# Kernel optimization log

Measured on AMD Instinct MI355X. Metric: run time of the kernel, lower is better.

Reference implementation:

```python
import jax, jax.numpy as jnp
import numpy as np

N, E = 50000, 640000
FEAT, EMB, HID, B = 128, 128, 512, 32


def setup_inputs() -> dict:
    key = jax.random.key(0)
    ks = jax.random.split(key, 12)
    def w(k, shape, fan_in):
        return jax.random.normal(k, shape, dtype=jnp.float32) / np.sqrt(fan_in)
    return {
        "x": jax.random.normal(ks[0], (N, FEAT), dtype=jnp.float32),
        "edge_index": jax.random.randint(ks[1], (2, E), 0, N, dtype=jnp.int64),
        "last_hidden": jax.random.normal(ks[2], (1, B, HID), dtype=jnp.float32),
        "W1_rel": w(ks[3], (FEAT, EMB), FEAT),
        "W1_root": w(ks[4], (FEAT, EMB), FEAT),
        "b1": jnp.zeros((EMB,), dtype=jnp.float32),
        "W2_rel": w(ks[5], (EMB, EMB), EMB),
        "W2_root": w(ks[6], (EMB, EMB), EMB),
        "b2": jnp.zeros((EMB,), dtype=jnp.float32),
        "Wp": w(ks[7], (HID, EMB), HID),
        "bp": jnp.zeros((EMB,), dtype=jnp.float32),
    }


def _rgcn(h, src, dst, W_rel, W_root, b):
    # transform-then-gather (N < E so cheaper): messages along edges src->dst
    msg = (h @ W_rel)[src]                                   # [E, emb]
    agg = jax.ops.segment_sum(msg, dst, num_segments=N)      # [N, emb]
    deg = jax.ops.segment_sum(jnp.ones((E,), h.dtype), dst, num_segments=N)
    agg = agg / jnp.maximum(deg, 1.0)[:, None]               # mean aggregation (PyG RGCNConv default)
    return agg + h @ W_root + b


def reference(x, edge_index, last_hidden, W1_rel, W1_root, b1, W2_rel, W2_root, b2, Wp, bp):
    src, dst = edge_index[0], edge_index[1]
    h = jax.nn.relu(_rgcn(x, src, dst, W1_rel, W1_root, b1))   # [N, emb]
    h = jax.nn.relu(_rgcn(h, src, dst, W2_rel, W2_root, b2))   # [N, emb]
    message_embed = (last_hidden @ Wp + bp)[0]                 # squeeze(0) -> [B, emb]
    scores = h @ message_embed.T                               # [N, B]
    return jax.nn.log_softmax(scores, axis=0)
```

## Files before the change

### kernel.cpp

```cpp
#include <hip/hip_runtime.h>
#include <hip/hip_bf16.h>

#define N_NODES 50000
#define N_EDGES 640000
#define DUMMY   N_NODES
#define PAD_SSRC 990000

typedef __attribute__((ext_vector_type(8))) short short8;
typedef __attribute__((ext_vector_type(4))) float floatx4;

__device__ __forceinline__ float bf2f(unsigned short u) {
    return __uint_as_float(((unsigned int)u) << 16);
}
__device__ __forceinline__ unsigned short f2bf(float x) {
    unsigned int u = __float_as_uint(x);
    u = (u + 0x7fffu + ((u >> 16) & 1u)) >> 16;
    return (unsigned short)u;
}
__device__ __forceinline__ unsigned char f2f8(float x) {
    int pk = __builtin_amdgcn_cvt_pk_fp8_f32(x, x, 0, false);
    return (unsigned char)(pk & 0xff);
}
__device__ __forceinline__ unsigned int pk4_fp8(float x0, float x1, float x2, float x3) {
    int v = __builtin_amdgcn_cvt_pk_fp8_f32(x0, x1, 0, false);
    v = __builtin_amdgcn_cvt_pk_fp8_f32(x2, x3, v, true);
    return (unsigned int)v;
}
__device__ __forceinline__ unsigned int pk2_bf16(float lo, float hi) {
    return (unsigned int)f2bf(lo) | ((unsigned int)f2bf(hi) << 16);
}

__global__ void __launch_bounds__(256) prep_k(const float* __restrict__ W0,
                                              const float* __restrict__ W1,
                                              const float* __restrict__ W2,
                                              const float* __restrict__ W3,
                                              unsigned short* __restrict__ T0,
                                              unsigned short* __restrict__ T1,
                                              unsigned short* __restrict__ T2,
                                              unsigned short* __restrict__ T3,
                                              int* __restrict__ cnt,
                                              const float* __restrict__ lh,
                                              const float* __restrict__ Wp,
                                              const float* __restrict__ bp,
                                              unsigned short* __restrict__ meb,
                                              unsigned short* __restrict__ ssrc,
                                              unsigned char* __restrict__ tbf,
                                              int* __restrict__ total,
                                              const int* __restrict__ dst,
                                              int* __restrict__ rank) {
    int b = blockIdx.x, tid = threadIdx.x;
    bool is_hist;
    int idx;
    if (b < 4414) { is_hist = ((b & 1) == 0); idx = b >> 1; }
    else          { is_hist = true;            idx = 2207 + (b - 4414); }
    if (is_hist) {
        int e = idx * 256 + tid;
        int d = dst[e];
        int r = atomicAdd(&cnt[d], 1);
        rank[e] = (r << 16) | d;
        return;
    }
    int s = idx;
    if (s < 256) {
        int i2 = s * 256 + tid;
        int w = i2 >> 14;
        int r = i2 & 16383;
        int n = r >> 7, k = r & 127;
        const float* W = (w == 0) ? W0 : (w == 1) ? W1 : (w == 2) ? W2 : W3;
        unsigned short* T = (w == 0) ? T0 : (w == 1) ? T1 : (w == 2) ? T2 : T3;
        T[r] = f2bf(W[k * 128 + n]);
    } else if (s < 272) {
        int o = (s - 256) * 256 + tid;
        int i = o >> 7, c = o & 127;
        float acc = bp[c];
        const float4* lr = (const float4*)(lh + i * 512);
        #pragma unroll 4
        for (int k4 = 0; k4 < 128; k4++) {
            float4 v = lr[k4];
            acc += v.x * Wp[(4 * k4 + 0) * 128 + c] + v.y * Wp[(4 * k4 + 1) * 128 + c]
                 + v.z * Wp[(4 * k4 + 2) * 128 + c] + v.w * Wp[(4 * k4 + 3) * 128 + c];
        }
        meb[o] = f2bf(acc);
    } else if (s < 2206) {
        int i = (s - 272) * 256 + tid;
        if (i < PAD_SSRC / 2) ((unsigned int*)ssrc)[i] = 0xC350C350u;
    } else {
        if (tid < 32) ((unsigned int*)(tbf + (size_t)DUMMY * 128))[tid] = 0;
        else if (tid == 32) *total = 0;
    }
}

#define EPI_LD 132
__device__ __forceinline__ void gemm_dual_body32(int bid, int tid, const short8 a[4],
                                                 const unsigned short* __restrict__ BtRel,
                                                 const unsigned short* __restrict__ BtRoot,
                                                 unsigned char* __restrict__ Trel,
                                                 unsigned short* __restrict__ Rootb,
                                                 int M, float* __restrict__ epi) {
    int wid = tid >> 6, lane = tid & 63;
    int rh = (wid >> 1) * 16;
    int ch = (wid & 1) * 64;
    int m = lane & 15, g = lane >> 4;
    floatx4 accR[4], accO[4];
    #pragma unroll
    for (int ct = 0; ct < 4; ct++) {
        accR[ct] = (floatx4)(0.f);
        accO[ct] = (floatx4)(0.f);
    }
    #pragma unroll
    for (int ct = 0; ct < 4; ct++) {
        const unsigned short* br = BtRel  + (size_t)(ch + ct * 16 + m) * 128 + g * 8;
        const unsigned short* bo = BtRoot + (size_t)(ch + ct * 16 + m) * 128 + g * 8;
        short8 bR[4], bO[4];
        #pragma unroll
        for (int kt = 0; kt < 4; kt++) {
            bR[kt] = *(const short8*)(br + kt * 32);
            bO[kt] = *(const short8*)(bo + kt * 32);
        }
        #pragma unroll
        for (int kt = 0; kt < 4; kt++) {
            accR[ct] = __builtin_amdgcn_mfma_f32_16x16x32_bf16(a[kt], bR[kt], accR[ct], 0, 0, 0);
            accO[ct] = __builtin_amdgcn_mfma_f32_16x16x32_bf16(a[kt], bO[kt], accO[ct], 0, 0, 0);
        }
    }
    int r0 = bid * 32;
    #pragma unroll
    for (int ct = 0; ct < 4; ct++)
        #pragma unroll
        for (int rg = 0; rg < 4; rg++)
            epi[(rh + g * 4 + rg) * EPI_LD + ch + ct * 16 + m] = accR[ct][rg];
    __syncthreads();
    {
        int lr = tid >> 3, c0 = (tid & 7) * 16;
        int ro = r0 + lr;
        const float* row = epi + lr * EPI_LD + c0;
        if (ro < M) {
            uint4 w;
            w.x = pk4_fp8(row[0],  row[1],  row[2],  row[3]);
            w.y = pk4_fp8(row[4],  row[5],  row[6],  row[7]);
            w.z = pk4_fp8(row[8],  row[9],  row[10], row[11]);
            w.w = pk4_fp8(row[12], row[13], row[14], row[15]);
            *(uint4*)(Trel + (size_t)ro * 128 + c0) = w;
        }
    }
    __syncthreads();
    #pragma unroll
    for (int ct = 0; ct < 4; ct++)
        #pragma unroll
        for (int rg = 0; rg < 4; rg++)
            epi[(rh + g * 4 + rg) * EPI_LD + ch + ct * 16 + m] = accO[ct][rg];
    __syncthreads();
    {
        int lr = tid >> 3, c0 = (tid & 7) * 16;
        int ro = r0 + lr;
        const float* row = epi + lr * EPI_LD + c0;
        if (ro < M) {
            uint4 w0, w1;
            w0.x = pk2_bf16(row[0],  row[1]);
            w0.y = pk2_bf16(row[2],  row[3]);
            w0.z = pk2_bf16(row[4],  row[5]);
            w0.w = pk2_bf16(row[6],  row[7]);
            w1.x = pk2_bf16(row[8],  row[9]);
            w1.y = pk2_bf16(row[10], row[11]);
            w1.z = pk2_bf16(row[12], row[13]);
            w1.w = pk2_bf16(row[14], row[15]);
            *(uint4*)(Rootb + (size_t)ro * 128 + c0) = w0;
            *(uint4*)(Rootb + (size_t)ro * 128 + c0 + 8) = w1;
        }
    }
}

__global__ void __launch_bounds__(256) allocgemm_k(const int* __restrict__ cnt,
                                                   int* __restrict__ prow,
                                                   int* __restrict__ total,
                                                   const float* __restrict__ A,
                                                   const unsigned short* __restrict__ BtRel,
                                                   const unsigned short* __restrict__ BtRoot,
                                                   unsigned char* __restrict__ Trel,
                                                   unsigned short* __restrict__ Rootb) {
    __shared__ float epi[32 * EPI_LD];
    __shared__ int sm[256];
    __shared__ int base_s;
    if (blockIdx.x < 196) {
        int t = threadIdx.x;
        int i = blockIdx.x * 256 + t;
        int pc = (i < N_NODES) ? ((cnt[i] + 7) & ~7) : 0;
        sm[t] = pc;
        __syncthreads();
        for (int off = 1; off < 256; off <<= 1) {
            int v = (t >= off) ? sm[t - off] : 0;
            __syncthreads();
            sm[t] += v;
            __syncthreads();
        }
        if (t == 255) base_s = atomicAdd(total, sm[255]);
        __syncthreads();
        if (i < N_NODES) prow[i] = base_s + sm[t] - pc;
    } else {
        int bid = blockIdx.x - 196, tid = threadIdx.x;
        int wid = tid >> 6, lane = tid & 63;
        int r0 = bid * 32 + (wid >> 1) * 16;
        int m = lane & 15, g = lane >> 4;
        int row = r0 + m;
        int rowc = (row < N_NODES) ? row : (N_NODES - 1);
        short8 a[4];
        #pragma unroll
        for (int kt = 0; kt < 4; kt++) {
            const float* p = A + (size_t)rowc * 128 + kt * 32 + g * 8;
            float4 v0 = *(const float4*)p;
            float4 v1 = *(const float4*)(p + 4);
            short8 t8;
            t8[0] = (short)f2bf(v0.x); t8[1] = (short)f2bf(v0.y);
            t8[2] = (short)f2bf(v0.z); t8[3] = (short)f2bf(v0.w);
            t8[4] = (short)f2bf(v1.x); t8[5] = (short)f2bf(v1.y);
            t8[6] = (short)f2bf(v1.z); t8[7] = (short)f2bf(v1.w);
            a[kt] = t8;
        }
        gemm_dual_body32(bid, tid, a, BtRel, BtRoot, Trel, Rootb, N_NODES, epi);
    }
}

__global__ void __launch_bounds__(256) place_k(const int* __restrict__ src,
                                               const int* __restrict__ prow,
                                               const int* __restrict__ rank,
                                               unsigned short* __restrict__ ssrc) {
    int e = blockIdx.x * 256 + threadIdx.x;
    if (e < N_EDGES) {
        int pk = rank[e];
        int d = pk & 0xffff;
        int r = pk >> 16;
        ssrc[prow[d] + r] = (unsigned short)src[e];
    }
}

__global__ void __launch_bounds__(256) gemm_dual_k(const unsigned short* __restrict__ A,
                                                   const unsigned short* __restrict__ BtRel,
                                                   const unsigned short* __restrict__ BtRoot,
                                                   unsigned char* __restrict__ Trel,
                                                   unsigned short* __restrict__ Rootb, int M) {
    __shared__ float epi[32 * EPI_LD];
    int tid = threadIdx.x;
    int wid = tid >> 6, lane = tid & 63;
    int r0 = blockIdx.x * 32 + (wid >> 1) * 16;
    int m = lane & 15, g = lane >> 4;
    int row = r0 + m;
    int rowc = (row < M) ? row : (M - 1);
    short8 a[4];
    #pragma unroll
    for (int kt = 0; kt < 4; kt++)
        a[kt] = *(const short8*)(A + (size_t)rowc * 128 + kt * 32 + g * 8);
    gemm_dual_body32(blockIdx.x, tid, a, BtRel, BtRoot, Trel, Rootb, M, epi);
}

__global__ void __launch_bounds__(256) agg_k(const int* __restrict__ prow,
                                             const int* __restrict__ cnt,
                                             const unsigned short* __restrict__ ssrc,
                                             const unsigned char* __restrict__ t,
                                             const unsigned short* __restrict__ rootb,
                                             const float* __restrict__ bias,
                                             unsigned short* __restrict__ hout) {
    int node = blockIdx.x * 4 + (threadIdx.x >> 6);
    if (node >= N_NODES) return;
    int lane = threadIdx.x & 63;
    int fl = lane & 31;
    int sh = (lane & 32) >> 1;
    int beg = prow[node];
    int deg = cnt[node];
    int endp = beg + ((deg + 7) & ~7);
    const unsigned char* tf = t + fl * 4;
    float a0=0.f,a1=0.f,a2=0.f,a3=0.f;
    float b0=0.f,b1=0.f,b2=0.f,b3=0.f;
    for (int e = beg; e < endp; e += 16) {
        uint4 w0 = *(const uint4*)(ssrc + e);
        uint4 w1 = (e + 8 < endp) ? *(const uint4*)(ssrc + e + 8)
                                  : make_uint4(0xC350C350u, 0xC350C350u, 0xC350C350u, 0xC350C350u);
        int i0 = (int)((w0.x >> sh) & 0xffffu);
        int i1 = (int)((w0.y >> sh) & 0xffffu);
        int i2 = (int)((w0.z >> sh) & 0xffffu);
        int i3 = (int)((w0.w >> sh) & 0xffffu);
        int i4 = (int)((w1.x >> sh) & 0xffffu);
        int i5 = (int)((w1.y >> sh) & 0xffffu);
        int i6 = (int)((w1.z >> sh) & 0xffffu);
        int i7 = (int)((w1.w >> sh) & 0xffffu);
        unsigned int u0 = *(const unsigned int*)(tf + (size_t)i0 * 128);
        unsigned int u1 = *(const unsigned int*)(tf + (size_t)i1 * 128);
        unsigned int u2 = *(const unsigned int*)(tf + (size_t)i2 * 128);
        unsigned int u3 = *(const unsigned int*)(tf + (size_t)i3 * 128);
        unsigned int u4 = *(const unsigned int*)(tf + (size_t)i4 * 128);
        unsigned int u5 = *(const unsigned int*)(tf + (size_t)i5 * 128);
        unsigned int u6 = *(const unsigned int*)(tf + (size_t)i6 * 128);
        unsigned int u7 = *(const unsigned int*)(tf + (size_t)i7 * 128);
        a0 += __builtin_amdgcn_cvt_f32_fp8(u0, 0) + __builtin_amdgcn_cvt_f32_fp8(u1, 0);
        a1 += __builtin_amdgcn_cvt_f32_fp8(u0, 1) + __builtin_amdgcn_cvt_f32_fp8(u1, 1);
        a2 += __builtin_amdgcn_cvt_f32_fp8(u0, 2) + __builtin_amdgcn_cvt_f32_fp8(u1, 2);
        a3 += __builtin_amdgcn_cvt_f32_fp8(u0, 3) + __builtin_amdgcn_cvt_f32_fp8(u1, 3);
        b0 += __builtin_amdgcn_cvt_f32_fp8(u2, 0) + __builtin_amdgcn_cvt_f32_fp8(u3, 0);
        b1 += __builtin_amdgcn_cvt_f32_fp8(u2, 1) + __builtin_amdgcn_cvt_f32_fp8(u3, 1);
        b2 += __builtin_amdgcn_cvt_f32_fp8(u2, 2) + __builtin_amdgcn_cvt_f32_fp8(u3, 2);
        b3 += __builtin_amdgcn_cvt_f32_fp8(u2, 3) + __builtin_amdgcn_cvt_f32_fp8(u3, 3);
        a0 += __builtin_amdgcn_cvt_f32_fp8(u4, 0) + __builtin_amdgcn_cvt_f32_fp8(u5, 0);
        a1 += __builtin_amdgcn_cvt_f32_fp8(u4, 1) + __builtin_amdgcn_cvt_f32_fp8(u5, 1);
        a2 += __builtin_amdgcn_cvt_f32_fp8(u4, 2) + __builtin_amdgcn_cvt_f32_fp8(u5, 2);
        a3 += __builtin_amdgcn_cvt_f32_fp8(u4, 3) + __builtin_amdgcn_cvt_f32_fp8(u5, 3);
        b0 += __builtin_amdgcn_cvt_f32_fp8(u6, 0) + __builtin_amdgcn_cvt_f32_fp8(u7, 0);
        b1 += __builtin_amdgcn_cvt_f32_fp8(u6, 1) + __builtin_amdgcn_cvt_f32_fp8(u7, 1);
        b2 += __builtin_amdgcn_cvt_f32_fp8(u6, 2) + __builtin_amdgcn_cvt_f32_fp8(u7, 2);
        b3 += __builtin_amdgcn_cvt_f32_fp8(u6, 3) + __builtin_amdgcn_cvt_f32_fp8(u7, 3);
    }
    a0 += b0; a1 += b1; a2 += b2; a3 += b3;
    a0 += __shfl_xor(a0, 32);
    a1 += __shfl_xor(a1, 32);
    a2 += __shfl_xor(a2, 32);
    a3 += __shfl_xor(a3, 32);
    if ((lane & 32) == 0) {
        float inv = 1.f / fmaxf((float)deg, 1.f);
        int f = fl * 4;
        ushort4 r = *(const ushort4*)(rootb + (size_t)node * 128 + f);
        float4 bb = *(const float4*)(bias + f);
        ushort4 o;
        o.x = f2bf(fmaxf(a0 * inv + bf2f(r.x) + bb.x, 0.f));
        o.y = f2bf(fmaxf(a1 * inv + bf2f(r.y) + bb.y, 0.f));
        o.z = f2bf(fmaxf(a2 * inv + bf2f(r.z) + bb.z, 0.f));
        o.w = f2bf(fmaxf(a3 * inv + bf2f(r.w) + bb.w, 0.f));
        *(ushort4*)(hout + (size_t)node * 128 + f) = o;
    }
}

__global__ void __launch_bounds__(256) scores_cs_k(const unsigned short* __restrict__ A,
                                                   const unsigned short* __restrict__ Bt,
                                                   float* __restrict__ S,
                                                   float* __restrict__ pm,
                                                   float* __restrict__ ps) {
    __shared__ float Sl[64][33];
    __shared__ float sm[256], ss[256];
    int tid = threadIdx.x;
    int wid = tid >> 6, lane = tid & 63;
    int r0 = blockIdx.x * 64 + wid * 16;
    int m = lane & 15, g = lane >> 4;
    int row = r0 + m;
    int rowc = (row < N_NODES) ? row : (N_NODES - 1);
    short8 a[4];
    #pragma unroll
    for (int kt = 0; kt < 4; kt++)
        a[kt] = *(const short8*)(A + (size_t)rowc * 128 + kt * 32 + g * 8);
    floatx4 acc[2];
    acc[0] = (floatx4)(0.f);
    acc[1] = (floatx4)(0.f);
    #pragma unroll
    for (int ct = 0; ct < 2; ct++) {
        const unsigned short* b = Bt + (size_t)(ct * 16 + m) * 128 + g * 8;
        #pragma unroll
        for (int kt = 0; kt < 4; kt++) {
            short8 bv = *(const short8*)(b + kt * 32);
            acc[ct] = __builtin_amdgcn_mfma_f32_16x16x32_bf16(a[kt], bv, acc[ct], 0, 0, 0);
        }
    }
    #pragma unroll
    for (int ct = 0; ct < 2; ct++) {
        #pragma unroll
        for (int rg = 0; rg < 4; rg++) {
            int lr = wid * 16 + g * 4 + rg;
            int ro = r0 + g * 4 + rg;
            Sl[lr][ct * 16 + m] = acc[ct][rg];
            if (ro < N_NODES) S[(size_t)ro * 32 + ct * 16 + m] = acc[ct][rg];
        }
    }
    __syncthreads();
    int col = tid & 31, sub = tid >> 5;
    int blkbase = blockIdx.x * 64;
    float mm = -3.4e38f, s = 0.f;
    for (int r = sub; r < 64; r += 8) {
        if (blkbase + r < N_NODES) {
            float v = Sl[r][col];
            if (v > mm) { s = s * __expf(mm - v) + 1.f; mm = v; }
            else        { s += __expf(v - mm); }
        }
    }
    sm[tid] = mm; ss[tid] = s;
    __syncthreads();
    for (int off = 128; off >= 32; off >>= 1) {
        if (tid < off) {
            float m2 = sm[tid + off], s2 = ss[tid + off];
            float M = fmaxf(sm[tid], m2);
            ss[tid] = ss[tid] * __expf(sm[tid] - M) + s2 * __expf(m2 - M);
            sm[tid] = M;
        }
        __syncthreads();
    }
    if (tid < 32) { pm[tid * 782 + blockIdx.x] = sm[tid]; ps[tid * 782 + blockIdx.x] = ss[tid]; }
}

__global__ void __launch_bounds__(256) merge_k(const float* __restrict__ pm,
                                               const float* __restrict__ ps,
                                               float* __restrict__ cmg,
                                               float* __restrict__ clg) {
    __shared__ float sm[256], ss[256];
    int col = blockIdx.x;
    int t = threadIdx.x;
    float m = -3.4e38f, s = 0.f;
    for (int c = t; c < 782; c += 256) {
        float m2 = pm[col * 782 + c], s2 = ps[col * 782 + c];
        float M = fmaxf(m, m2);
        s = s * __expf(m - M) + s2 * __expf(m2 - M);
        m = M;
    }
    sm[t] = m; ss[t] = s;
    __syncthreads();
    for (int off = 128; off > 0; off >>= 1) {
        if (t < off) {
            float m2 = sm[t + off], s2 = ss[t + off];
            float M = fmaxf(sm[t], m2);
            ss[t] = ss[t] * __expf(sm[t] - M) + s2 * __expf(m2 - M);
            sm[t] = M;
        }
        __syncthreads();
    }
    if (t == 0) { cmg[col] = sm[0]; clg[col] = logf(ss[0]); }
}

__global__ void __launch_bounds__(256) final_k(const float* __restrict__ S,
                                               const float* __restrict__ cmg,
                                               const float* __restrict__ clg,
                                               float* __restrict__ out) {
    __shared__ float cc[32];
    int t = threadIdx.x;
    if (t < 32) cc[t] = cmg[t] + clg[t];
    __syncthreads();
    int idx = blockIdx.x * 256 + t;
    if (idx < N_NODES * 32) {
        int b = idx & 31;
        out[idx] = S[idx] - cc[b];
    }
}

extern "C" void kernel_launch(void* const* d_in, const int* in_sizes, int n_in,
                              void* d_out, int out_size, void* d_ws, size_t ws_size,
                              hipStream_t stream) {
    const float* x       = (const float*)d_in[0];
    const int*   ei      = (const int*)d_in[1];
    const float* lh      = (const float*)d_in[2];
    const float* W1_rel  = (const float*)d_in[3];
    const float* W1_root = (const float*)d_in[4];
    const float* b1      = (const float*)d_in[5];
    const float* W2_rel  = (const float*)d_in[6];
    const float* W2_root = (const float*)d_in[7];
    const float* b2      = (const float*)d_in[8];
    const float* Wp      = (const float*)d_in[9];
    const float* bp      = (const float*)d_in[10];
    float* out = (float*)d_out;
    float* ws  = (float*)d_ws;

    unsigned char*  tbf   = (unsigned char*)(ws + 3200000);
    unsigned short* rootb = (unsigned short*)(ws + 4800032);
    unsigned short* hb    = (unsigned short*)(ws + 8000032);
    unsigned short* Wt1r  = (unsigned short*)(ws + 11200032);
    unsigned short* Wt1o  = (unsigned short*)(ws + 11208224);
    unsigned short* Wt2r  = (unsigned short*)(ws + 11216416);
    unsigned short* Wt2o  = (unsigned short*)(ws + 11224608);
    unsigned short* MEb   = (unsigned short*)(ws + 11232800);
    float* pm   = ws + 11234848;
    float* ps   = ws + 11259872;
    float* cmg  = ws + 11284896;
    float* clg  = ws + 11284928;
    int*   cnt  = (int*)(ws + 11284960);
    int*   prow = (int*)(ws + 11334960);
    int*   total= (int*)(ws + 11384961);
    int*   rank = (int*)(ws + 11384964);
    unsigned short* ssrc = (unsigned short*)(ws + 12024964);
    float* S    = ws + 12519964;

    const int* srcp = ei;
    const int* dstp = ei + N_EDGES;

    const int e_grid   = (N_EDGES + 255) / 256;
    const int ew_grid  = (N_NODES * 32 + 255) / 256;
    const int agg_grid = (N_NODES + 3) / 4;
    const int mm_grid  = (N_NODES + 63) / 64;
    const int g32_grid = (N_NODES + 31) / 32;

    hipMemsetAsync(cnt, 0, N_NODES * sizeof(int), stream);

    prep_k<<<4707, 256, 0, stream>>>(W1_rel, W1_root, W2_rel, W2_root,
                                     Wt1r, Wt1o, Wt2r, Wt2o,
                                     cnt, lh, Wp, bp, MEb, ssrc, tbf, total,
                                     dstp, rank);

    allocgemm_k<<<196 + g32_grid, 256, 0, stream>>>(cnt, prow, total,
                                                    x, Wt1r, Wt1o, tbf, rootb);

    place_k<<<e_grid, 256, 0, stream>>>(srcp, prow, rank, ssrc);

    agg_k<<<agg_grid, 256, 0, stream>>>(prow, cnt, ssrc, tbf, rootb, b1, hb);

    gemm_dual_k<<<g32_grid, 256, 0, stream>>>(hb, Wt2r, Wt2o, tbf, rootb, N_NODES);

    agg_k<<<agg_grid, 256, 0, stream>>>(prow, cnt, ssrc, tbf, rootb, b2, hb);

    scores_cs_k<<<mm_grid, 256, 0, stream>>>(hb, MEb, S, pm, ps);

    merge_k<<<32, 256, 0, stream>>>(pm, ps, cmg, clg);

    final_k<<<ew_grid, 256, 0, stream>>>(S, cmg, clg, out);
}
```

Before: 256.6 us.

## Stage GEMM A and B tiles through swizzled LDS instead of per-lane global loads

The dual GEMM now loads A tiles and the transposed weight matrices cooperatively into a shared-memory pool with an XOR swizzle. MFMA operands are then read from LDS, where before each wave fetched its B fragments straight from global memory. The Rel and Root weights are staged one after the other in the same buffer, which is also reused for the epilogue. The intent is coalesced, shared loads of the weights. In exchange it adds barriers and a 40KB LDS footprint, which may lower occupancy.

```diff
diff --git a/kernel.cpp b/kernel.cpp
--- a/kernel.cpp
+++ b/kernel.cpp
@@ -91,39 +91,95 @@
 }
 
 #define EPI_LD 132
-__device__ __forceinline__ void gemm_dual_body32(int bid, int tid, const short8 a[4],
-                                                 const unsigned short* __restrict__ BtRel,
-                                                 const unsigned short* __restrict__ BtRoot,
-                                                 unsigned char* __restrict__ Trel,
-                                                 unsigned short* __restrict__ Rootb,
-                                                 int M, float* __restrict__ epi) {
+template <bool AF32>
+__device__ __forceinline__ void gemm_dual_lds32(int bid, int tid,
+                                                const void* __restrict__ Ain,
+                                                const unsigned short* __restrict__ BtRel,
+                                                const unsigned short* __restrict__ BtRoot,
+                                                unsigned char* __restrict__ Trel,
+                                                unsigned short* __restrict__ Rootb,
+                                                int M, char* __restrict__ pool) {
     int wid = tid >> 6, lane = tid & 63;
-    int rh = (wid >> 1) * 16;
-    int ch = (wid & 1) * 64;
     int m = lane & 15, g = lane >> 4;
+    int r0 = bid * 32;
+    if constexpr (AF32) {
+        const float* A = (const float*)Ain;
+        #pragma unroll
+        for (int j = 0; j < 2; j++) {
+            int k = j * 256 + tid;
+            int row = k >> 4;
+            int grow = r0 + row; grow = (grow < M) ? grow : (M - 1);
+            const float* p = A + (size_t)grow * 128 + (k & 15) * 8;
+            float4 v0 = *(const float4*)p;
+            float4 v1 = *(const float4*)(p + 4);
+            short8 t8;
+            t8[0] = (short)f2bf(v0.x); t8[1] = (short)f2bf(v0.y);
+            t8[2] = (short)f2bf(v0.z); t8[3] = (short)f2bf(v0.w);
+            t8[4] = (short)f2bf(v1.x); t8[5] = (short)f2bf(v1.y);
+            t8[6] = (short)f2bf(v1.z); t8[7] = (short)f2bf(v1.w);
+            *(short8*)(pool + ((k * 16) ^ ((row & 7) << 4))) = t8;
+        }
+    } else {
+        const unsigned short* A = (const unsigned short*)Ain;
+        #pragma unroll
+        for (int j = 0; j < 2; j++) {
+            int k = j * 256 + tid;
+            int row = k >> 4;
+            int grow = r0 + row; grow = (grow < M) ? grow : (M - 1);
+            short8 v = *(const short8*)(A + (size_t)grow * 128 + (k & 15) * 8);
+            *(short8*)(pool + ((k * 16) ^ ((row & 7) << 4))) = v;
+        }
+    }
+    #pragma unroll
+    for (int j = 0; j < 8; j++) {
+        int k = j * 256 + tid;
+        int row = k >> 4;
+        short8 v = *(const short8*)(BtRel + (size_t)k * 8);
+        *(short8*)(pool + 8192 + ((k * 16) ^ ((row & 7) << 4))) = v;
+    }
+    __syncthreads();
+    int lrow = (wid >> 1) * 16 + m;
+    int asw = (lrow & 7) << 4, abase = lrow * 256;
+    short8 a[4];
+    #pragma unroll
+    for (int kt = 0; kt < 4; kt++)
+        a[kt] = *(const short8*)(pool + ((abase + kt * 64 + g * 16) ^ asw));
+    int browbase = (wid & 1) * 64;
     floatx4 accR[4], accO[4];
     #pragma unroll
     for (int ct = 0; ct < 4; ct++) {
         accR[ct] = (floatx4)(0.f);
+        int brow = browbase + ct * 16 + m;
+        int bbase = brow * 256, bsw = (brow & 7) << 4;
+        #pragma unroll
+        for (int kt = 0; kt < 4; kt++) {
+            short8 bv = *(const short8*)(pool + 8192 + ((bbase + kt * 64 + g * 16) ^ bsw));
+            accR[ct] = __builtin_amdgcn_mfma_f32_16x16x32_bf16(a[kt], bv, accR[ct], 0, 0, 0);
+        }
+    }
+    __syncthreads();
+    #pragma unroll
+    for (int j = 0; j < 8; j++) {
+        int k = j * 256 + tid;
+        int row = k >> 4;
+        short8 v = *(const short8*)(BtRoot + (size_t)k * 8);
+        *(short8*)(pool + 8192 + ((k * 16) ^ ((row & 7) << 4))) = v;
+    }
+    __syncthreads();
+    #pragma unroll
+    for (int ct = 0; ct < 4; ct++) {
         accO[ct] = (floatx4)(0.f);
-    }
-    #pragma unroll
-    for (int ct = 0; ct < 4; ct++) {
-        const unsigned short* br = BtRel  + (size_t)(ch + ct * 16 + m) * 128 + g * 8;
-        const unsigned short* bo = BtRoot + (size_t)(ch + ct * 16 + m) * 128 + g * 8;
-        short8 bR[4], bO[4];
+        int brow = browbase + ct * 16 + m;
+        int bbase = brow * 256, bsw = (brow & 7) << 4;
         #pragma unroll
         for (int kt = 0; kt < 4; kt++) {
-            bR[kt] = *(const short8*)(br + kt * 32);
-            bO[kt] = *(const short8*)(bo + kt * 32);
-        }
-        #pragma unroll
-        for (int kt = 0; kt < 4; kt++) {
-            accR[ct] = __builtin_amdgcn_mfma_f32_16x16x32_bf16(a[kt], bR[kt], accR[ct], 0, 0, 0);
-            accO[ct] = __builtin_amdgcn_mfma_f32_16x16x32_bf16(a[kt], bO[kt], accO[ct], 0, 0, 0);
-        }
-    }
-    int r0 = bid * 32;
+            short8 bv = *(const short8*)(pool + 8192 + ((bbase + kt * 64 + g * 16) ^ bsw));
+            accO[ct] = __builtin_amdgcn_mfma_f32_16x16x32_bf16(a[kt], bv, accO[ct], 0, 0, 0);
+        }
+    }
+    __syncthreads();
+    float* epi = (float*)(pool + 8192);
+    int rh = (wid >> 1) * 16, ch = (wid & 1) * 64;
     #pragma unroll
     for (int ct = 0; ct < 4; ct++)
         #pragma unroll
@@ -178,10 +234,10 @@
                                                    const unsigned short* __restrict__ BtRoot,
                                                    unsigned char* __restrict__ Trel,
                                                    unsigned short* __restrict__ Rootb) {
-    __shared__ float epi[32 * EPI_LD];
-    __shared__ int sm[256];
-    __shared__ int base_s;
+    __shared__ __align__(16) char pool[40960];
     if (blockIdx.x < 196) {
+        int* sm = (int*)pool;
+        int* base_s = (int*)(pool + 1024);
         int t = threadIdx.x;
         int i = blockIdx.x * 256 + t;
         int pc = (i < N_NODES) ? ((cnt[i] + 7) & ~7) : 0;
@@ -193,30 +249,12 @@
             sm[t] += v;
             __syncthreads();
         }
-        if (t == 255) base_s = atomicAdd(total, sm[255]);
+        if (t == 255) *base_s = atomicAdd(total, sm[255]);
         __syncthreads();
-        if (i < N_NODES) prow[i] = base_s + sm[t] - pc;
+        if (i < N_NODES) prow[i] = *base_s + sm[t] - pc;
     } else {
-        int bid = blockIdx.x - 196, tid = threadIdx.x;
-        int wid = tid >> 6, lane = tid & 63;
-        int r0 = bid * 32 + (wid >> 1) * 16;
-        int m = lane & 15, g = lane >> 4;
-        int row = r0 + m;
-        int rowc = (row < N_NODES) ? row : (N_NODES - 1);
-        short8 a[4];
-        #pragma unroll
-        for (int kt = 0; kt < 4; kt++) {
-            const float* p = A + (size_t)rowc * 128 + kt * 32 + g * 8;
-            float4 v0 = *(const float4*)p;
-            float4 v1 = *(const float4*)(p + 4);
-            short8 t8;
-            t8[0] = (short)f2bf(v0.x); t8[1] = (short)f2bf(v0.y);
-            t8[2] = (short)f2bf(v0.z); t8[3] = (short)f2bf(v0.w);
-            t8[4] = (short)f2bf(v1.x); t8[5] = (short)f2bf(v1.y);
-            t8[6] = (short)f2bf(v1.z); t8[7] = (short)f2bf(v1.w);
-            a[kt] = t8;
-        }
-        gemm_dual_body32(bid, tid, a, BtRel, BtRoot, Trel, Rootb, N_NODES, epi);
+        gemm_dual_lds32<true>(blockIdx.x - 196, threadIdx.x, A, BtRel, BtRoot,
+                              Trel, Rootb, N_NODES, pool);
     }
 }
 
@@ -238,18 +276,8 @@
                                                    const unsigned short* __restrict__ BtRoot,
                                                    unsigned char* __restrict__ Trel,
                                                    unsigned short* __restrict__ Rootb, int M) {
-    __shared__ float epi[32 * EPI_LD];
-    int tid = threadIdx.x;
-    int wid = tid >> 6, lane = tid & 63;
-    int r0 = blockIdx.x * 32 + (wid >> 1) * 16;
-    int m = lane & 15, g = lane >> 4;
-    int row = r0 + m;
-    int rowc = (row < M) ? row : (M - 1);
-    short8 a[4];
-    #pragma unroll
-    for (int kt = 0; kt < 4; kt++)
-        a[kt] = *(const short8*)(A + (size_t)rowc * 128 + kt * 32 + g * 8);
-    gemm_dual_body32(blockIdx.x, tid, a, BtRel, BtRoot, Trel, Rootb, M, epi);
+    __shared__ __align__(16) char pool[40960];
+    gemm_dual_lds32<false>(blockIdx.x, threadIdx.x, A, BtRel, BtRoot, Trel, Rootb, M, pool);
 }
 
 __global__ void __launch_bounds__(256) agg_k(const int* __restrict__ prow,
```

Measured after the change: 216.8 us (median of 2 runs). 15.5% less time.
